# Performance work log

Hardware: AMD Instinct MI355X
Metric: run time of the kernel (lower is better)

Reference implementation:

```python
import jax, jax.numpy as jnp
import numpy as np

B, T, TM = 4, 1024, 1500
D_MODEL, D_FFN, H, D_HEAD, D_MEM = 1024, 4096, 16, 64, 1024
EPS = 1e-5


def layernorm(x, g):
    m = jnp.mean(x, axis=-1, keepdims=True)
    xc = x - m
    v = jnp.mean(xc * xc, axis=-1, keepdims=True)
    return xc * jax.lax.rsqrt(v + EPS) * g


def setup_inputs() -> dict:
    key = jax.random.key(0)
    ks = jax.random.split(key, 12)
    s = lambda fan_in: 1.0 / np.sqrt(fan_in)
    return {
        "x": jax.random.normal(ks[0], (B, T, D_MODEL), jnp.float32),
        "encoder_output": jax.random.normal(ks[1], (B, TM, D_MEM), jnp.float32),
        "encoder_mask": jax.random.randint(ks[2], (B, TM), 0, 2).astype(bool),
        "w_qkv": jax.random.normal(ks[3], (D_MODEL, 3 * H * D_HEAD), jnp.float32) * s(D_MODEL),
        "w_o_sa": jax.random.normal(ks[4], (H * D_HEAD, D_MODEL), jnp.float32) * s(H * D_HEAD),
        "w_q": jax.random.normal(ks[5], (D_MODEL, H * D_HEAD), jnp.float32) * s(D_MODEL),
        "w_kv": jax.random.normal(ks[6], (D_MEM, 2 * H * D_HEAD), jnp.float32) * s(D_MEM),
        "w_o_xa": jax.random.normal(ks[7], (H * D_HEAD, D_MODEL), jnp.float32) * s(H * D_HEAD),
        "w_ff1": jax.random.normal(ks[8], (D_MODEL, D_FFN), jnp.float32) * s(D_MODEL),
        "w_ff2": jax.random.normal(ks[9], (D_FFN, D_MODEL), jnp.float32) * s(D_FFN),
        "g_sa": jnp.ones((D_MODEL,), jnp.float32),
        "g_xaq": jnp.ones((D_MODEL,), jnp.float32),
        "g_xam": jnp.ones((D_MEM,), jnp.float32),
        "g_ff": jnp.ones((D_MODEL,), jnp.float32),
    }


def reference(x, encoder_output, encoder_mask, w_qkv, w_o_sa, w_q, w_kv, w_o_xa,
              w_ff1, w_ff2, g_sa, g_xaq, g_xam, g_ff):
    b, t, _ = x.shape
    scale = D_HEAD ** -0.5

    # ---- causal self-attention ----
    residual = x
    xn = layernorm(x, g_sa)
    qkv = (xn @ w_qkv).reshape(b, t, 3, H, D_HEAD)
    q, k, v = qkv[:, :, 0], qkv[:, :, 1], qkv[:, :, 2]  # (B,T,H,D)
    scores = jnp.einsum('bqhd,bkhd->bhqk', q, k) * scale
    causal = jnp.tril(jnp.ones((t, t), x.dtype))
    scores = scores + (1.0 - causal) * -1e9
    attn = jax.nn.softmax(scores, axis=-1)
    sa = jnp.einsum('bhqk,bkhd->bqhd', attn, v).reshape(b, t, H * D_HEAD)
    x = residual + sa @ w_o_sa

    # ---- cross-attention ----
    residual = x
    qn = layernorm(x, g_xaq)
    mn = layernorm(encoder_output, g_xam)
    tq, tm = t, mn.shape[1]
    qx = (qn @ w_q).reshape(b, tq, H, D_HEAD)
    kvx = (mn @ w_kv).reshape(b, tm, 2, H, D_HEAD)
    kx, vx = kvx[:, :, 0], kvx[:, :, 1]
    xs = jnp.einsum('bqhd,bkhd->bhqk', qx, kx) * scale
    xs = jnp.where(encoder_mask[:, None, None, :], xs, -jnp.inf)
    xattn = jax.nn.softmax(xs, axis=-1)
    xa = jnp.einsum('bhqk,bkhd->bqhd', xattn, vx).reshape(b, tq, H * D_HEAD)
    x = residual + xa @ w_o_xa

    # ---- pointwise FFN (kernel_size=1 conv == linear) ----
    residual = x
    h = layernorm(x, g_ff)
    h = jax.nn.gelu(h @ w_ff1, approximate=True) @ w_ff2
    x = residual + h
    return (x, k, v)
```

## Files before the change

### kernel.cpp

```cpp
#include <hip/hip_runtime.h>
#include <hip/hip_bf16.h>
#include <cstdint>
#include <cstddef>


typedef __attribute__((ext_vector_type(4))) float f32x4;
typedef __attribute__((ext_vector_type(8))) short s8v;
typedef __attribute__((ext_vector_type(2))) unsigned uint2v;

#define DEVI __device__ __forceinline__

DEVI short f2bf(float f) {
  union { float f; unsigned u; } x; x.f = f;
  unsigned r = x.u + 0x7fffu + ((x.u >> 16) & 1u);
  return (short)(r >> 16);
}
DEVI float bf2f(short s) {
  union { unsigned u; float f; } x; x.u = ((unsigned)(unsigned short)s) << 16;
  return x.f;
}
DEVI unsigned cvtpk_bf2(float lo, float hi) {
  unsigned r;
  asm("v_cvt_pk_bf16_f32 %0, %1, %2" : "=v"(r) : "v"(lo), "v"(hi));
  return r;
}
DEVI float fexp2(float x) {
  float r;
  asm("v_exp_f32 %0, %1" : "=v"(r) : "v"(x));
  return r;
}
DEVI float bpermf(int srclane, float v) {
  union { float f; int i; } x; x.f = v;
  x.i = __builtin_amdgcn_ds_bpermute(srclane << 2, x.i);
  return x.f;
}
DEVI void gload_lds16(const void* g, void* l) {
  __builtin_amdgcn_global_load_lds((const __attribute__((address_space(1))) void*)g,
                                   (__attribute__((address_space(3))) void*)l,
                                   16, 0, 0);
}

__global__ __launch_bounds__(256) void k_transpose_cvt(
    const float* __restrict__ w, short* __restrict__ wt, int K, int N) {
  __shared__ float tile[32][33];
  int n0 = blockIdx.x * 32, k0 = blockIdx.y * 32;
  int tx = threadIdx.x & 31, ty = threadIdx.x >> 5;
#pragma unroll
  for (int i = 0; i < 32; i += 8)
    tile[ty + i][tx] = w[(size_t)(k0 + ty + i) * N + n0 + tx];
  __syncthreads();
#pragma unroll
  for (int i = 0; i < 32; i += 8)
    wt[(size_t)(n0 + ty + i) * K + k0 + tx] = f2bf(tile[tx][ty + i]);
}

__global__ __launch_bounds__(256) void k_vtrans(
    const short* __restrict__ src, int srs, int coff,
    short* __restrict__ dst, int T, int Tp) {
  __shared__ short tile[32][72];
  int bh = blockIdx.y, b = bh >> 4, h = bh & 15;
  int t0 = blockIdx.x * 32;
  const short* sB = src + (size_t)b * T * srs + coff + h * 64;
  short* dB = dst + (size_t)bh * 64 * Tp;
  int t = threadIdx.x;
  int r = t >> 3, c = (t & 7) * 8;
  int tr = t0 + r; if (tr > T - 1) tr = T - 1;
  *(s8v*)&tile[r][c] = *(const s8v*)(sB + (size_t)tr * srs + c);
  __syncthreads();
  int d = t & 63, ch = t >> 6;
  s8v o;
#pragma unroll
  for (int j = 0; j < 8; j++) o[j] = tile[ch * 8 + j][d];
  *(s8v*)(dB + (size_t)d * Tp + t0 + ch * 8) = o;
}

__global__ void k_maskpack(const int* __restrict__ mask,
                           unsigned long long* __restrict__ out, int Tk, int mw) {
  int b = blockIdx.x, w = threadIdx.x;
  if (w >= mw) return;
  unsigned long long v = 0;
  const int* mb = mask + (size_t)b * Tk;
#pragma unroll 4
  for (int j = 0; j < 64; j++) {
    int k = w * 64 + j;
    if (k < Tk && mb[k]) v |= (1ull << j);
  }
  out[(size_t)b * mw + w] = v;
}

__global__ __launch_bounds__(256) void k_ln(
    const float* __restrict__ x, const float* __restrict__ g,
    short* __restrict__ out) {
  int row = blockIdx.x;
  const float* xr = x + (size_t)row * 1024;
  int t = threadIdx.x, wid = t >> 6, lane = t & 63;
  f32x4 v = ((const f32x4*)xr)[t];
  float s = v[0] + v[1] + v[2] + v[3];
#pragma unroll
  for (int m = 32; m >= 1; m >>= 1) s += __shfl_xor(s, m);
  __shared__ float red[4];
  if (lane == 0) red[wid] = s;
  __syncthreads();
  float mean = (red[0] + red[1] + red[2] + red[3]) * (1.f / 1024.f);
  float q = 0.f;
#pragma unroll
  for (int i = 0; i < 4; i++) { v[i] -= mean; q += v[i] * v[i]; }
#pragma unroll
  for (int m = 32; m >= 1; m >>= 1) q += __shfl_xor(q, m);
  __syncthreads();
  if (lane == 0) red[wid] = q;
  __syncthreads();
  float var = (red[0] + red[1] + red[2] + red[3]) * (1.f / 1024.f);
  float rs = rsqrtf(var + 1e-5f);
  f32x4 gv = ((const f32x4*)g)[t];
  unsigned w0 = cvtpk_bf2(v[0] * rs * gv[0], v[1] * rs * gv[1]);
  unsigned w1 = cvtpk_bf2(v[2] * rs * gv[2], v[3] * rs * gv[3]);
  uint2v w = {w0, w1};
  *(uint2v*)(out + (size_t)row * 1024 + t * 4) = w;
}

template <bool GELU_, bool F32OUT, bool BF16OUT, bool KV>
__global__ __launch_bounds__(256) void k_gemm3(
    const short* __restrict__ A, const short* __restrict__ Bt,
    float* __restrict__ Cf, short* __restrict__ Cb,
    float* __restrict__ okv, int M, int N, int K, int lda, int ldb) {
  __shared__ short As[128 * 64];
  __shared__ short Bs[128 * 64];
  int z = blockIdx.z;
  A += (size_t)z * K;
  Bt += (size_t)z * K;
  if (F32OUT) Cf += (size_t)z * (size_t)M * N;

  int bx, by;
  {
    int gx = gridDim.x, gy = gridDim.y;
    int nxy = gx * gy, chunk = nxy >> 3;
    int orig = blockIdx.y * gx + blockIdx.x;
    int gid = (orig & 7) * chunk + (orig >> 3);
    int full = gy << 3, nfull = gx >> 3, lim = nfull * full;
    if (gid < lim) {
      int band = gid / full, r = gid - band * full;
      bx = (band << 3) + (r & 7);
      by = r >> 3;
    } else {
      int r = gid - lim, w = gx - (nfull << 3);
      bx = (nfull << 3) + r % w;
      by = r / w;
    }
  }
  int am = bx * 128, bn = by * 128;

  int t = threadIdx.x, wid = t >> 6, lane = t & 63;
  int la = lane & 15, lb = lane >> 4;
  int wr = wid >> 1, wc = wid & 1;

  const short* gp[8];
  int dof[8];
#pragma unroll
  for (int l = 0; l < 8; l++) {
    int cl = (l & 3) * 256 + t;
    int row = cl >> 3, g = cl & 7;
    int col = (g ^ (row & 7)) << 3;
    if (l < 4) {
      int ar = am + row; if (ar > M - 1) ar = M - 1;
      gp[l] = A + (size_t)ar * lda + col;
    } else {
      gp[l] = Bt + (size_t)(bn + row) * ldb + col;
    }
    dof[l] = ((l & 3) * 256 + wid * 64) * 8;
  }

  int aOff[4], bOff[4];
#pragma unroll
  for (int m = 0; m < 4; m++) {
    int r = wr * 64 + m * 16 + la;
    aOff[m] = r * 64 + ((lb ^ (r & 7)) << 3);
  }
#pragma unroll
  for (int n = 0; n < 4; n++) {
    int r = wc * 64 + n * 16 + la;
    bOff[n] = r * 64 + ((lb ^ (r & 7)) << 3);
  }

  f32x4 acc[4][4];
#pragma unroll
  for (int m = 0; m < 4; m++)
#pragma unroll
    for (int n = 0; n < 4; n++) acc[m][n] = (f32x4){0.f, 0.f, 0.f, 0.f};

  int nk = K >> 6;
  for (int ks = 0; ks < nk; ++ks) {
#pragma unroll
    for (int l = 0; l < 4; l++) { gload_lds16(gp[l], As + dof[l]); gp[l] += 64; }
#pragma unroll
    for (int l = 4; l < 8; l++) { gload_lds16(gp[l], Bs + dof[l]); gp[l] += 64; }
    __syncthreads();
#pragma unroll
    for (int kk = 0; kk < 2; kk++) {
      s8v af[4], bfg[4];
#pragma unroll
      for (int m = 0; m < 4; m++)
        af[m] = *(const s8v*)(As + (aOff[m] ^ (kk << 5)));
#pragma unroll
      for (int n = 0; n < 4; n++)
        bfg[n] = *(const s8v*)(Bs + (bOff[n] ^ (kk << 5)));
#pragma unroll
      for (int m = 0; m < 4; m++)
#pragma unroll
        for (int n = 0; n < 4; n++)
          acc[m][n] = __builtin_amdgcn_mfma_f32_16x16x32_bf16(af[m], bfg[n], acc[m][n], 0, 0, 0);
    }
    __syncthreads();
  }

#pragma unroll
  for (int m = 0; m < 4; m++) {
    int rb = am + wr * 64 + m * 16 + lb * 4;
#pragma unroll
    for (int n = 0; n < 4; n++) {
      int col = bn + wc * 64 + n * 16 + la;
#pragma unroll
      for (int j = 0; j < 4; j++) {
        int r = rb + j;
        if (r < M) {
          float v = acc[m][n][j];
          if (GELU_) {
            float u = v;
            float y = 0.7978845608f * u * (1.f + 0.044715f * u * u);
            float e = fexp2(fminf(y * 2.88539008f, 80.f));
            float th = (e - 1.f) * __builtin_amdgcn_rcpf(e + 1.f);
            v = 0.5f * u * (1.f + th);
          }
          if (F32OUT) Cf[(size_t)r * N + col] = v;
          if (BF16OUT) Cb[(size_t)r * N + col] = f2bf(v);
          if (KV) {
            if (col >= 2048)
              okv[(size_t)4096 * 1024 + (size_t)r * 1024 + (col - 2048)] = v;
            else if (col >= 1024)
              okv[(size_t)r * 1024 + (col - 1024)] = v;
          }
        }
      }
    }
  }
}

template <bool RESID, bool BF16O>
__global__ __launch_bounds__(256) void k_red2(
    const f32x4* __restrict__ p, const f32x4* __restrict__ res,
    float* __restrict__ outf, short* __restrict__ outb, int n) {
  int i = blockIdx.x * 256 + threadIdx.x;
  f32x4 v = p[i] + p[i + (size_t)n];
  if (RESID) v += res[i];
  if (BF16O) {
    uint2v w = {cvtpk_bf2(v[0], v[1]), cvtpk_bf2(v[2], v[3])};
    *(uint2v*)(outb + (size_t)i * 4) = w;
  } else {
    *(f32x4*)(outf + (size_t)i * 4) = v;
  }
}

template <bool CAUSAL>
__global__ __launch_bounds__(512) void k_attn4(
    const short* __restrict__ qbuf, int qrs,
    const short* __restrict__ kbuf, int krs,
    const short* __restrict__ vT, int vts,
    short* __restrict__ obuf, int ors,
    const unsigned long long* __restrict__ mbits, int mwords,
    int Tq, int Tk, float scale) {
  __shared__ short Ks[64 * 64];
  __shared__ short Vs[64 * 64];
  __shared__ short Ps[8 * 1024];
  int bh = blockIdx.y, b = bh >> 4, h = bh & 15;
  int t = threadIdx.x, wid = t >> 6, lane = t & 63;
  int la = lane & 15, lb = lane >> 4;
  float lscale = scale * 1.44269504f;

  const short* qB = qbuf + (size_t)b * Tq * qrs + h * 64;
  const short* kB = kbuf + (size_t)b * Tk * krs + h * 64;
  const short* vB = vT + (size_t)bh * 64 * vts;
  char* Pw = (char*)(Ps + wid * 1024);

  int sr = t >> 3, scol = (t & 7) * 8;
  int swz = sr * 64 + (scol ^ ((sr & 7) << 3));

  int nsup = CAUSAL ? 2 : 1;
  for (int s = 0; s < nsup; s++) {
    int st = CAUSAL ? (s ? 7 - blockIdx.x : blockIdx.x) : blockIdx.x;
    int q0 = st * 128 + wid * 16;
    int nkt = CAUSAL ? 2 * st + 2 : (Tk + 63) >> 6;
    int lastkt = CAUSAL ? (q0 >> 6) : nkt - 1;

    s8v qf[2];
#pragma unroll
    for (int kk = 0; kk < 2; kk++)
      qf[kk] = *(const s8v*)(qB + (size_t)(q0 + la) * qrs + kk * 32 + lb * 8);

    f32x4 accO[4];
#pragma unroll
    for (int n = 0; n < 4; n++) accO[n] = (f32x4){0.f, 0.f, 0.f, 0.f};
    float m = -1e30f, l = 0.f;

    s8v krg, vrg;
    {
      int tk = sr; if (tk > Tk - 1) tk = Tk - 1;
      krg = *(const s8v*)(kB + (size_t)tk * krs + scol);
      vrg = *(const s8v*)(vB + (size_t)sr * vts + scol);
    }

    for (int kt = 0; kt < nkt; kt++) {
      int kb0 = kt << 6;
      __syncthreads();
      *(s8v*)&Ks[swz] = krg;
      *(s8v*)&Vs[swz] = vrg;
      __syncthreads();
      if (kt + 1 < nkt) {
        int kb = kb0 + 64;
        int tk = kb + sr; if (tk > Tk - 1) tk = Tk - 1;
        krg = *(const s8v*)(kB + (size_t)tk * krs + scol);
        vrg = *(const s8v*)(vB + (size_t)sr * vts + kb + scol);
      }
      if (kt > lastkt) continue;

      bool needMask;
      unsigned long long wm = ~0ull;
      if (CAUSAL) {
        needMask = (kt == lastkt);
      } else {
        wm = mbits[(size_t)b * mwords + kt];
        needMask = (wm != ~0ull);
      }

      float sc[4][4];
      __builtin_amdgcn_s_setprio(1);
#pragma unroll
      for (int n = 0; n < 4; n++) {
        f32x4 a = (f32x4){0.f, 0.f, 0.f, 0.f};
#pragma unroll
        for (int kk = 0; kk < 2; kk++) {
          s8v kf = *(const s8v*)&Ks[(n * 16 + la) * 64 +
                                    ((kk * 32 + lb * 8) ^ ((la & 7) << 3))];
          a = __builtin_amdgcn_mfma_f32_16x16x32_bf16(kf, qf[kk], a, 0, 0, 0);
        }
#pragma unroll
        for (int j = 0; j < 4; j++) {
          float sv = a[j] * lscale;
          if (needMask) {
            int ki = n * 16 + lb * 4 + j;
            bool ok = CAUSAL ? (kb0 + ki <= q0 + la) : (((wm >> ki) & 1ull) != 0);
            sv = ok ? sv : -1e30f;
          }
          sc[n][j] = sv;
        }
      }
      __builtin_amdgcn_s_setprio(0);

      float tm = sc[0][0];
#pragma unroll
      for (int n = 0; n < 4; n++)
#pragma unroll
        for (int j = 0; j < 4; j++) tm = fmaxf(tm, sc[n][j]);
      tm = fmaxf(tm, __shfl_xor(tm, 16));
      tm = fmaxf(tm, __shfl_xor(tm, 32));
      tm = fmaxf(tm, -1e4f);

      bool skip = __all(tm - m <= 10.f);
      float alpha = 1.f;
      if (!skip) {
        float mn_ = fmaxf(m, tm);
        alpha = fexp2(m - mn_);
        m = mn_;
      }

      unsigned W[4][2];
      float ps = 0.f;
#pragma unroll
      for (int n = 0; n < 4; n++) {
        float p0 = fexp2(sc[n][0] - m), p1 = fexp2(sc[n][1] - m);
        float p2 = fexp2(sc[n][2] - m), p3 = fexp2(sc[n][3] - m);
        ps += (p0 + p1) + (p2 + p3);
        W[n][0] = cvtpk_bf2(p0, p1);
        W[n][1] = cvtpk_bf2(p2, p3);
      }
      ps += __shfl_xor(ps, 16);
      ps += __shfl_xor(ps, 32);
      l = l * alpha + ps;

      if (!skip) {
#pragma unroll
        for (int j = 0; j < 4; j++) {
          float aj = bpermf(lb * 20 + j, alpha);
#pragma unroll
          for (int n = 0; n < 4; n++) accO[n][j] *= aj;
        }
      }

#pragma unroll
      for (int n = 0; n < 4; n++) {
        uint2v w2 = {W[n][0], W[n][1]};
        *(uint2v*)(Pw + ((la * 128 + n * 32 + lb * 8) ^ ((la & 7) << 4))) = w2;
      }
      __builtin_amdgcn_s_setprio(1);
#pragma unroll
      for (int kk = 0; kk < 2; kk++) {
        s8v pa = *(const s8v*)(Pw + ((la * 128 + kk * 64 + lb * 16) ^ ((la & 7) << 4)));
#pragma unroll
        for (int n = 0; n < 4; n++) {
          s8v vf = *(const s8v*)&Vs[(n * 16 + la) * 64 +
                                    ((kk * 32 + lb * 8) ^ ((la & 7) << 3))];
          accO[n] = __builtin_amdgcn_mfma_f32_16x16x32_bf16(pa, vf, accO[n], 0, 0, 0);
        }
      }
      __builtin_amdgcn_s_setprio(0);
    }

#pragma unroll
    for (int j = 0; j < 4; j++) {
      float lj = bpermf(lb * 20 + j, l);
      float inv = 1.f / lj;
      int r = q0 + lb * 4 + j;
#pragma unroll
      for (int n = 0; n < 4; n++)
        obuf[(size_t)(b * Tq + r) * ors + h * 64 + n * 16 + la] = f2bf(accO[n][j] * inv);
    }
  }
}

extern "C" void kernel_launch(void* const* d_in, const int* in_sizes, int n_in,
                              void* d_out, int out_size, void* d_ws, size_t ws_size,
                              hipStream_t stream) {
  (void)in_sizes; (void)n_in; (void)out_size; (void)ws_size;
  const float* x      = (const float*)d_in[0];
  const float* enc    = (const float*)d_in[1];
  const int*   mask   = (const int*)d_in[2];
  const float* w_qkv  = (const float*)d_in[3];
  const float* w_o_sa = (const float*)d_in[4];
  const float* w_q    = (const float*)d_in[5];
  const float* w_kv   = (const float*)d_in[6];
  const float* w_o_xa = (const float*)d_in[7];
  const float* w_ff1  = (const float*)d_in[8];
  const float* w_ff2  = (const float*)d_in[9];
  const float* g_sa   = (const float*)d_in[10];
  const float* g_xaq  = (const float*)d_in[11];
  const float* g_xam  = (const float*)d_in[12];
  const float* g_ff   = (const float*)d_in[13];

  float* out_x = (float*)d_out;
  float* out_k = out_x + (size_t)4096 * 1024;

  char* ws = (char*)d_ws;
  size_t off = 0;
  auto alloc = [&](size_t bytes) -> void* {
    void* p = ws + off;
    off += (bytes + 255) & ~(size_t)255;
    return p;
  };
  short* wqkv_t = (short*)alloc((size_t)3072 * 1024 * 2);
  short* wosa_t = (short*)alloc((size_t)1024 * 1024 * 2);
  short* wq_t   = (short*)alloc((size_t)1024 * 1024 * 2);
  short* wkv_t  = (short*)alloc((size_t)2048 * 1024 * 2);
  short* woxa_t = (short*)alloc((size_t)1024 * 1024 * 2);
  short* wff1_t = (short*)alloc((size_t)4096 * 1024 * 2);
  short* wff2_t = (short*)alloc((size_t)1024 * 4096 * 2);
  short* xn     = (short*)alloc((size_t)4096 * 1024 * 2);
  short* qkv_b  = (short*)alloc((size_t)4096 * 3072 * 2);
  short* sa_b   = (short*)alloc((size_t)4096 * 1024 * 2);
  float* x1     = (float*)alloc((size_t)4096 * 1024 * 4);
  short* qn     = (short*)alloc((size_t)4096 * 1024 * 2);
  short* mn     = (short*)alloc((size_t)6000 * 1024 * 2);
  short* qx_b   = (short*)alloc((size_t)4096 * 1024 * 2);
  short* kvx_b  = (short*)alloc((size_t)6000 * 2048 * 2);
  short* xa_b   = (short*)alloc((size_t)4096 * 1024 * 2);
  float* x2     = (float*)alloc((size_t)4096 * 1024 * 4);
  short* hn     = (short*)alloc((size_t)4096 * 1024 * 2);
  short* h1     = (short*)alloc((size_t)4096 * 4096 * 2);
  unsigned long long* mbits = (unsigned long long*)alloc(4 * 24 * 8);

  short* vTsa = xn;
  short* vTxa = h1;
  float* partH = (float*)h1;
  float* partQ = (float*)qkv_b;
  const int NRED = 1048576;

  k_transpose_cvt<<<dim3(96, 32), 256, 0, stream>>>(w_qkv, wqkv_t, 1024, 3072);
  k_transpose_cvt<<<dim3(32, 32), 256, 0, stream>>>(w_o_sa, wosa_t, 1024, 1024);
  k_transpose_cvt<<<dim3(32, 32), 256, 0, stream>>>(w_q, wq_t, 1024, 1024);
  k_transpose_cvt<<<dim3(64, 32), 256, 0, stream>>>(w_kv, wkv_t, 1024, 2048);
  k_transpose_cvt<<<dim3(32, 32), 256, 0, stream>>>(w_o_xa, woxa_t, 1024, 1024);
  k_transpose_cvt<<<dim3(128, 32), 256, 0, stream>>>(w_ff1, wff1_t, 1024, 4096);
  k_transpose_cvt<<<dim3(32, 128), 256, 0, stream>>>(w_ff2, wff2_t, 4096, 1024);
  k_maskpack<<<4, 64, 0, stream>>>(mask, mbits, 1500, 24);

  k_ln<<<4096, 256, 0, stream>>>(x, g_sa, xn);
  k_gemm3<false, false, true, true><<<dim3(32, 24), 256, 0, stream>>>(
      xn, wqkv_t, nullptr, qkv_b, out_k, 4096, 3072, 1024, 1024, 1024);
  k_vtrans<<<dim3(32, 64), 256, 0, stream>>>(qkv_b, 3072, 2048, vTsa, 1024, 1024);
  k_attn4<true><<<dim3(4, 64), 512, 0, stream>>>(
      qkv_b, 3072, qkv_b + 1024, 3072, vTsa, 1024,
      sa_b, 1024, nullptr, 0, 1024, 1024, 0.125f);
  k_gemm3<false, true, false, false><<<dim3(32, 8, 2), 256, 0, stream>>>(
      sa_b, wosa_t, partH, nullptr, nullptr, 4096, 1024, 512, 1024, 1024);
  k_red2<true, false><<<4096, 256, 0, stream>>>(
      (const f32x4*)partH, (const f32x4*)x, x1, nullptr, NRED);

  k_ln<<<4096, 256, 0, stream>>>(x1, g_xaq, qn);
  k_ln<<<6000, 256, 0, stream>>>(enc, g_xam, mn);
  k_gemm3<false, true, false, false><<<dim3(32, 8, 2), 256, 0, stream>>>(
      qn, wq_t, partH, nullptr, nullptr, 4096, 1024, 512, 1024, 1024);
  k_red2<false, true><<<4096, 256, 0, stream>>>(
      (const f32x4*)partH, nullptr, nullptr, qx_b, NRED);
  k_gemm3<false, false, true, false><<<dim3(47, 16), 256, 0, stream>>>(
      mn, wkv_t, nullptr, kvx_b, nullptr, 6000, 2048, 1024, 1024, 1024);
  k_vtrans<<<dim3(48, 64), 256, 0, stream>>>(kvx_b, 2048, 1024, vTxa, 1500, 1536);
  k_attn4<false><<<dim3(8, 64), 512, 0, stream>>>(
      qx_b, 1024, kvx_b, 2048, vTxa, 1536,
      xa_b, 1024, mbits, 24, 1024, 1500, 0.125f);
  k_gemm3<false, true, false, false><<<dim3(32, 8, 2), 256, 0, stream>>>(
      xa_b, woxa_t, partH, nullptr, nullptr, 4096, 1024, 512, 1024, 1024);
  k_red2<true, false><<<4096, 256, 0, stream>>>(
      (const f32x4*)partH, (const f32x4*)x1, x2, nullptr, NRED);

  k_ln<<<4096, 256, 0, stream>>>(x2, g_ff, hn);
  k_gemm3<true, false, true, false><<<dim3(32, 32), 256, 0, stream>>>(
      hn, wff1_t, nullptr, h1, nullptr, 4096, 4096, 1024, 1024, 1024);
  k_gemm3<false, true, false, false><<<dim3(32, 8, 2), 256, 0, stream>>>(
      h1, wff2_t, partQ, nullptr, nullptr, 4096, 1024, 2048, 4096, 4096);
  k_red2<true, false><<<4096, 256, 0, stream>>>(
      (const f32x4*)partQ, (const f32x4*)x2, out_x, nullptr, NRED);
}
```

Before: 436.8 us.

## Fuse residual-reduce with layernorm, fold FFN2 residual, remap attention grid, vectorize weight transpose

Result: slower. 465.8 us (+6.6%).

```diff
diff --git a/kernel.cpp b/kernel.cpp
--- a/kernel.cpp
+++ b/kernel.cpp
@@ -15,10 +15,6 @@
   unsigned r = x.u + 0x7fffu + ((x.u >> 16) & 1u);
   return (short)(r >> 16);
 }
-DEVI float bf2f(short s) {
-  union { unsigned u; float f; } x; x.u = ((unsigned)(unsigned short)s) << 16;
-  return x.f;
-}
 DEVI unsigned cvtpk_bf2(float lo, float hi) {
   unsigned r;
   asm("v_cvt_pk_bf16_f32 %0, %1, %2" : "=v"(r) : "v"(lo), "v"(hi));
@@ -44,14 +40,14 @@
     const float* __restrict__ w, short* __restrict__ wt, int K, int N) {
   __shared__ float tile[32][33];
   int n0 = blockIdx.x * 32, k0 = blockIdx.y * 32;
-  int tx = threadIdx.x & 31, ty = threadIdx.x >> 5;
-#pragma unroll
-  for (int i = 0; i < 32; i += 8)
-    tile[ty + i][tx] = w[(size_t)(k0 + ty + i) * N + n0 + tx];
-  __syncthreads();
-#pragma unroll
-  for (int i = 0; i < 32; i += 8)
-    wt[(size_t)(n0 + ty + i) * K + k0 + tx] = f2bf(tile[tx][ty + i]);
+  int t = threadIdx.x;
+  int row = t >> 3, c4 = (t & 7) * 4;
+  *(f32x4*)&tile[row][c4] = *(const f32x4*)(w + (size_t)(k0 + row) * N + n0 + c4);
+  __syncthreads();
+  float v0 = tile[c4 + 0][row], v1 = tile[c4 + 1][row];
+  float v2 = tile[c4 + 2][row], v3 = tile[c4 + 3][row];
+  uint2v o = {cvtpk_bf2(v0, v1), cvtpk_bf2(v2, v3)};
+  *(uint2v*)(wt + (size_t)(n0 + row) * K + k0 + c4) = o;
 }
 
 __global__ __launch_bounds__(256) void k_vtrans(
@@ -119,17 +115,18 @@
   *(uint2v*)(out + (size_t)row * 1024 + t * 4) = w;
 }
 
-template <bool GELU_, bool F32OUT, bool BF16OUT, bool KV>
+template <bool RES, bool GELU_, bool F32OUT, bool BF16OUT, bool KV>
 __global__ __launch_bounds__(256) void k_gemm3(
     const short* __restrict__ A, const short* __restrict__ Bt,
     float* __restrict__ Cf, short* __restrict__ Cb,
-    float* __restrict__ okv, int M, int N, int K, int lda, int ldb) {
+    const float* __restrict__ res, float* __restrict__ okv,
+    int M, int N, int K, int lda, int ldb) {
   __shared__ short As[128 * 64];
   __shared__ short Bs[128 * 64];
   int z = blockIdx.z;
   A += (size_t)z * K;
   Bt += (size_t)z * K;
-  if (F32OUT) Cf += (size_t)z * (size_t)M * N;
+  if (F32OUT && !RES) Cf += (size_t)z * (size_t)M * N;
 
   int bx, by;
   {
@@ -224,6 +221,7 @@
         int r = rb + j;
         if (r < M) {
           float v = acc[m][n][j];
+          if (RES) v += res[(size_t)r * N + col];
           if (GELU_) {
             float u = v;
             float y = 0.7978845608f * u * (1.f + 0.044715f * u * u);
@@ -245,19 +243,44 @@
   }
 }
 
-template <bool RESID, bool BF16O>
-__global__ __launch_bounds__(256) void k_red2(
-    const f32x4* __restrict__ p, const f32x4* __restrict__ res,
-    float* __restrict__ outf, short* __restrict__ outb, int n) {
+__global__ __launch_bounds__(256) void k_red2b(
+    const f32x4* __restrict__ p, short* __restrict__ outb, int n) {
   int i = blockIdx.x * 256 + threadIdx.x;
   f32x4 v = p[i] + p[i + (size_t)n];
-  if (RESID) v += res[i];
-  if (BF16O) {
-    uint2v w = {cvtpk_bf2(v[0], v[1]), cvtpk_bf2(v[2], v[3])};
-    *(uint2v*)(outb + (size_t)i * 4) = w;
-  } else {
-    *(f32x4*)(outf + (size_t)i * 4) = v;
-  }
+  uint2v w = {cvtpk_bf2(v[0], v[1]), cvtpk_bf2(v[2], v[3])};
+  *(uint2v*)(outb + (size_t)i * 4) = w;
+}
+
+__global__ __launch_bounds__(256) void k_red2ln(
+    const f32x4* __restrict__ p, const f32x4* __restrict__ res,
+    float* __restrict__ xout, short* __restrict__ nout,
+    const float* __restrict__ g, int n) {
+  int row = blockIdx.x;
+  int t = threadIdx.x, wid = t >> 6, lane = t & 63;
+  size_t i = (size_t)row * 256 + t;
+  f32x4 v = res[i] + (p[i] + p[i + (size_t)n]);
+  ((f32x4*)xout)[i] = v;
+  float s = v[0] + v[1] + v[2] + v[3];
+#pragma unroll
+  for (int m = 32; m >= 1; m >>= 1) s += __shfl_xor(s, m);
+  __shared__ float red[4];
+  if (lane == 0) red[wid] = s;
+  __syncthreads();
+  float mean = (red[0] + red[1] + red[2] + red[3]) * (1.f / 1024.f);
+  float q = 0.f;
+#pragma unroll
+  for (int k = 0; k < 4; k++) { v[k] -= mean; q += v[k] * v[k]; }
+#pragma unroll
+  for (int m = 32; m >= 1; m >>= 1) q += __shfl_xor(q, m);
+  __syncthreads();
+  if (lane == 0) red[wid] = q;
+  __syncthreads();
+  float var = (red[0] + red[1] + red[2] + red[3]) * (1.f / 1024.f);
+  float rs = rsqrtf(var + 1e-5f);
+  f32x4 gv = ((const f32x4*)g)[t];
+  uint2v w = {cvtpk_bf2(v[0] * rs * gv[0], v[1] * rs * gv[1]),
+              cvtpk_bf2(v[2] * rs * gv[2], v[3] * rs * gv[3])};
+  *(uint2v*)(nout + (size_t)row * 1024 + t * 4) = w;
 }
 
 template <bool CAUSAL>
@@ -271,7 +294,11 @@
   __shared__ short Ks[64 * 64];
   __shared__ short Vs[64 * 64];
   __shared__ short Ps[8 * 1024];
-  int bh = blockIdx.y, b = bh >> 4, h = bh & 15;
+  int lid = blockIdx.y * gridDim.x + blockIdx.x;
+  int rest = lid >> 3;
+  int bh = (lid & 7) * 8 + (rest & 7);
+  int qsel = rest >> 3;
+  int b = bh >> 4, h = bh & 15;
   int t = threadIdx.x, wid = t >> 6, lane = t & 63;
   int la = lane & 15, lb = lane >> 4;
   float lscale = scale * 1.44269504f;
@@ -286,7 +313,7 @@
 
   int nsup = CAUSAL ? 2 : 1;
   for (int s = 0; s < nsup; s++) {
-    int st = CAUSAL ? (s ? 7 - blockIdx.x : blockIdx.x) : blockIdx.x;
+    int st = CAUSAL ? (s ? 7 - qsel : qsel) : qsel;
     int q0 = st * 128 + wid * 16;
     int nkt = CAUSAL ? 2 * st + 2 : (Tk + 63) >> 6;
     int lastkt = CAUSAL ? (q0 >> 6) : nkt - 1;
@@ -479,7 +506,6 @@
   short* vTsa = xn;
   short* vTxa = h1;
   float* partH = (float*)h1;
-  float* partQ = (float*)qkv_b;
   const int NRED = 1048576;
 
   k_transpose_cvt<<<dim3(96, 32), 256, 0, stream>>>(w_qkv, wqkv_t, 1024, 3072);
@@ -492,39 +518,34 @@
   k_maskpack<<<4, 64, 0, stream>>>(mask, mbits, 1500, 24);
 
   k_ln<<<4096, 256, 0, stream>>>(x, g_sa, xn);
-  k_gemm3<false, false, true, true><<<dim3(32, 24), 256, 0, stream>>>(
-      xn, wqkv_t, nullptr, qkv_b, out_k, 4096, 3072, 1024, 1024, 1024);
+  k_gemm3<false, false, false, true, true><<<dim3(32, 24), 256, 0, stream>>>(
+      xn, wqkv_t, nullptr, qkv_b, nullptr, out_k, 4096, 3072, 1024, 1024, 1024);
   k_vtrans<<<dim3(32, 64), 256, 0, stream>>>(qkv_b, 3072, 2048, vTsa, 1024, 1024);
   k_attn4<true><<<dim3(4, 64), 512, 0, stream>>>(
       qkv_b, 3072, qkv_b + 1024, 3072, vTsa, 1024,
       sa_b, 1024, nullptr, 0, 1024, 1024, 0.125f);
-  k_gemm3<false, true, false, false><<<dim3(32, 8, 2), 256, 0, stream>>>(
-      sa_b, wosa_t, partH, nullptr, nullptr, 4096, 1024, 512, 1024, 1024);
-  k_red2<true, false><<<4096, 256, 0, stream>>>(
-      (const f32x4*)partH, (const f32x4*)x, x1, nullptr, NRED);
-
-  k_ln<<<4096, 256, 0, stream>>>(x1, g_xaq, qn);
+  k_gemm3<false, false, true, false, false><<<dim3(32, 8, 2), 256, 0, stream>>>(
+      sa_b, wosa_t, partH, nullptr, nullptr, nullptr, 4096, 1024, 512, 1024, 1024);
+  k_red2ln<<<4096, 256, 0, stream>>>(
+      (const f32x4*)partH, (const f32x4*)x, x1, qn, g_xaq, NRED);
+
   k_ln<<<6000, 256, 0, stream>>>(enc, g_xam, mn);
-  k_gemm3<false, true, false, false><<<dim3(32, 8, 2), 256, 0, stream>>>(
-      qn, wq_t, partH, nullptr, nullptr, 4096, 1024, 512, 1024, 1024);
-  k_red2<false, true><<<4096, 256, 0, stream>>>(
-      (const f32x4*)partH, nullptr, nullptr, qx_b, NRED);
-  k_gemm3<false, false, true, false><<<dim3(47, 16), 256, 0, stream>>>(
-      mn, wkv_t, nullptr, kvx_b, nullptr, 6000, 2048, 1024, 1024, 1024);
+  k_gemm3<false, false, true, false, false><<<dim3(32, 8, 2), 256, 0, stream>>>(
+      qn, wq_t, partH, nullptr, nullptr, nullptr, 4096, 1024, 512, 1024, 1024);
+  k_red2b<<<4096, 256, 0, stream>>>((const f32x4*)partH, qx_b, NRED);
+  k_gemm3<false, false, false, true, false><<<dim3(47, 16), 256, 0, stream>>>(
+      mn, wkv_t, nullptr, kvx_b, nullptr, nullptr, 6000, 2048, 1024, 1024, 1024);
   k_vtrans<<<dim3(48, 64), 256, 0, stream>>>(kvx_b, 2048, 1024, vTxa, 1500, 1536);
   k_attn4<false><<<dim3(8, 64), 512, 0, stream>>>(
       qx_b, 1024, kvx_b, 2048, vTxa, 1536,
       xa_b, 1024, mbits, 24, 1024, 1500, 0.125f);
-  k_gemm3<false, true, false, false><<<dim3(32, 8, 2), 256, 0, stream>>>(
-      xa_b, woxa_t, partH, nullptr, nullptr, 4096, 1024, 512, 1024, 1024);
-  k_red2<true, false><<<4096, 256, 0, stream>>>(
-      (const f32x4*)partH, (const f32x4*)x1, x2, nullptr, NRED);
-
-  k_ln<<<4096, 256, 0, stream>>>(x2, g_ff, hn);
-  k_gemm3<true, false, true, false><<<dim3(32, 32), 256, 0, stream>>>(
-      hn, wff1_t, nullptr, h1, nullptr, 4096, 4096, 1024, 1024, 1024);
-  k_gemm3<false, true, false, false><<<dim3(32, 8, 2), 256, 0, stream>>>(
-      h1, wff2_t, partQ, nullptr, nullptr, 4096, 1024, 2048, 4096, 4096);
-  k_red2<true, false><<<4096, 256, 0, stream>>>(
-      (const f32x4*)partQ, (const f32x4*)x2, out_x, nullptr, NRED);
-}
+  k_gemm3<false, false, true, false, false><<<dim3(32, 8, 2), 256, 0, stream>>>(
+      xa_b, woxa_t, partH, nullptr, nullptr, nullptr, 4096, 1024, 512, 1024, 1024);
+  k_red2ln<<<4096, 256, 0, stream>>>(
+      (const f32x4*)partH, (const f32x4*)x1, x2, hn, g_ff, NRED);
+
+  k_gemm3<false, true, false, true, false><<<dim3(32, 32), 256, 0, stream>>>(
+      hn, wff1_t, nullptr, h1, nullptr, nullptr, 4096, 4096, 1024, 1024, 1024);
+  k_gemm3<true, false, true, false, false><<<dim3(32, 8), 256, 0, stream>>>(
+      h1, wff2_t, out_x, nullptr, x2, nullptr, 4096, 1024, 4096, 4096, 4096);
+}
```
